# Performance work log

Measured on AMD Instinct MI355X. Metric: run time of the kernel, lower is better.

The kernel has to match this reference:

```python
import jax, jax.numpy as jnp
import numpy as np

B, L, D = 4, 8192, 1024

def setup_inputs() -> dict:
    key = jax.random.key(0)
    kx, kg, kc = jax.random.split(key, 3)
    scale = 1.0 / np.sqrt(D)  # ~xavier for [D,D]
    return {
        "x": jax.random.normal(kx, (B, L, D), dtype=jnp.float32),
        "Wg": jax.random.normal(kg, (D, D), dtype=jnp.float32) * scale,
        "bg": jnp.ones((D,), dtype=jnp.float32),   # gate bias init = 1.0
        "Wc": jax.random.normal(kc, (D, D), dtype=jnp.float32) * scale,
        "bc": jnp.zeros((D,), dtype=jnp.float32),  # candidate bias init = 0
    }

def _mingru_scan(gates, candidates):
    # Linear recurrence h_t = g_t * h_{t-1} + c_t, h_0 = 0, along axis=1 (L).
    # Associative combine for pairs (a, b) representing h -> a*h + b.
    def combine(e1, e2):
        a1, b1 = e1
        a2, b2 = e2
        return a2 * a1, a2 * b1 + b2
    _, h = jax.lax.associative_scan(combine, (gates, candidates), axis=1)
    return h

def reference(x, Wg, bg, Wc, bc):
    # gate_proj / candidate_proj: y = x @ W.T + b (torch Linear convention)
    gates = jax.nn.sigmoid(jnp.einsum('bld,ed->ble', x, Wg) + bg)
    candidates = jnp.tanh(jnp.einsum('bld,ed->ble', x, Wc) + bc)
    return _mingru_scan(gates, candidates)  # dropout=0 -> identity
```

## Files before the change

kernel.cpp:

```cpp
#include <hip/hip_runtime.h>
#include <math.h>

#define B_ 4
#define L_ 8192
#define D_ 1024
#define M_ (B_ * L_)
#define K_ D_

#define BM 128
#define BN 128
#define BK 32

#define NCH 64
#define CHL 128

typedef short bf16x8 __attribute__((ext_vector_type(8)));
typedef float f32x4 __attribute__((ext_vector_type(4)));

__device__ __forceinline__ unsigned short f2bf(float f) {
    unsigned u = __float_as_uint(f);
    u += 0x7fff + ((u >> 16) & 1);
    return (unsigned short)(u >> 16);
}
__device__ __forceinline__ float bf2f(unsigned short h) {
    return __uint_as_float(((unsigned)h) << 16);
}

__device__ __forceinline__ void async16(const void* g, void* l) {
    __builtin_amdgcn_global_load_lds(
        (const __attribute__((address_space(1))) unsigned int*)g,
        (__attribute__((address_space(3))) unsigned int*)l, 16, 0, 0);
}

__global__ __launch_bounds__(256) void wprep_kernel(
    const float* __restrict__ Wg, const float* __restrict__ Wc,
    unsigned short* __restrict__ Wghi, unsigned short* __restrict__ Wglo,
    unsigned short* __restrict__ Wchi, unsigned short* __restrict__ Wclo)
{
    int idx = (blockIdx.x * 256 + threadIdx.x) * 4;
    const int n = D_ * D_;
    const float* src; unsigned short *dh, *dl; int o;
    if (idx < n) { src = Wg; dh = Wghi; dl = Wglo; o = idx; }
    else         { src = Wc; dh = Wchi; dl = Wclo; o = idx - n; }
    float4 v = *(const float4*)(src + o);
    ushort4 hi, lo;
    hi.x = f2bf(v.x); lo.x = f2bf(v.x - bf2f(hi.x));
    hi.y = f2bf(v.y); lo.y = f2bf(v.y - bf2f(hi.y));
    hi.z = f2bf(v.z); lo.z = f2bf(v.z - bf2f(hi.z));
    hi.w = f2bf(v.w); lo.w = f2bf(v.w - bf2f(hi.w));
    *(ushort4*)(dh + o) = hi;
    *(ushort4*)(dl + o) = lo;
}

__global__ __launch_bounds__(256) void xprep_kernel(
    const float* __restrict__ X,
    unsigned short* __restrict__ Xhi, unsigned short* __restrict__ Xlo)
{
    size_t idx = ((size_t)blockIdx.x * 256 + threadIdx.x) * 4;
    float4 v = *(const float4*)(X + idx);
    ushort4 hi, lo;
    hi.x = f2bf(v.x); lo.x = f2bf(v.x - bf2f(hi.x));
    hi.y = f2bf(v.y); lo.y = f2bf(v.y - bf2f(hi.y));
    hi.z = f2bf(v.z); lo.z = f2bf(v.z - bf2f(hi.z));
    hi.w = f2bf(v.w); lo.w = f2bf(v.w - bf2f(hi.w));
    *(ushort4*)(Xhi + idx) = hi;
    *(ushort4*)(Xlo + idx) = lo;
}

__global__ __launch_bounds__(256, 2) void gemm_scan_kernel(
    const unsigned short* __restrict__ Xhi, const unsigned short* __restrict__ Xlo,
    const unsigned short* __restrict__ Wghi, const unsigned short* __restrict__ Wglo,
    const unsigned short* __restrict__ Wchi, const unsigned short* __restrict__ Wclo,
    const float* __restrict__ bg, const float* __restrict__ bc,
    float* __restrict__ P_ws, float* __restrict__ h_ws,
    float* __restrict__ carryA, float* __restrict__ carryB)
{
    __shared__ __align__(16) unsigned short sAhi[BM * BK];
    __shared__ __align__(16) unsigned short sAlo[BM * BK];
    __shared__ __align__(16) unsigned short sB[2][4][BN * BK];

    const int t = threadIdx.x;
    const int lane = t & 63;
    const int w = t >> 6;
    const int wrow = w >> 1;
    const int wcol = w & 1;
    const int quad = lane >> 4;
    const int l16  = lane & 15;

    const int m0 = blockIdx.x * BM;
    const int n0 = blockIdx.y * BN;

    const int stRow = t >> 2;
    const int stKc  = (t & 3) << 3;
    const int stO   = t * 16;

    f32x4 accg[4][4] = {};
    f32x4 accc[4][4] = {};

    unsigned short* sBc = &sB[0][0][0];
    unsigned short* sBn = &sB[1][0][0];

#pragma unroll
    for (int p = 0; p < 2; ++p) {
        const int o = stO + p * 4096;
        const size_t gb = (size_t)(n0 + stRow + p * 64) * K_ + stKc;
        async16(Wghi + gb, (char*)sBc + o);
        async16(Wglo + gb, (char*)sBc + 8192 + o);
        async16(Wchi + gb, (char*)sBc + 16384 + o);
        async16(Wclo + gb, (char*)sBc + 24576 + o);
    }

#pragma unroll 1
    for (int s = 0; s < 32; ++s) {
        const int k0 = s * BK;

        __builtin_amdgcn_s_barrier();

#pragma unroll
        for (int p = 0; p < 2; ++p) {
            const int o = stO + p * 4096;
            const size_t ga = (size_t)(m0 + stRow + p * 64) * K_ + k0 + stKc;
            async16(Xhi + ga, (char*)sAhi + o);
            async16(Xlo + ga, (char*)sAlo + o);
        }

        if (s < 31) {
#pragma unroll
            for (int p = 0; p < 2; ++p) {
                const int o = stO + p * 4096;
                const size_t gb = (size_t)(n0 + stRow + p * 64) * K_ + (k0 + BK) + stKc;
                async16(Wghi + gb, (char*)sBn + o);
                async16(Wglo + gb, (char*)sBn + 8192 + o);
                async16(Wchi + gb, (char*)sBn + 16384 + o);
                async16(Wclo + gb, (char*)sBn + 24576 + o);
            }
            asm volatile("s_waitcnt vmcnt(8)" ::: "memory");
        } else {
            asm volatile("s_waitcnt vmcnt(0)" ::: "memory");
        }
        __builtin_amdgcn_sched_barrier(0);

        __builtin_amdgcn_s_barrier();

        bf16x8 ahi[4], alo[4];
#pragma unroll
        for (int i = 0; i < 4; ++i) {
            const int off = (wrow * 64 + i * 16 + l16) * BK + quad * 8;
            ahi[i] = *(const bf16x8*)(sAhi + off);
            alo[i] = *(const bf16x8*)(sAlo + off);
        }
        __builtin_amdgcn_s_setprio(1);
#pragma unroll
        for (int j = 0; j < 4; ++j) {
            const int off = (wcol * 64 + j * 16 + l16) * BK + quad * 8;
            bf16x8 bgh = *(const bf16x8*)(sBc + off);
            bf16x8 bgl = *(const bf16x8*)(sBc + 4096 + off);
            bf16x8 bch = *(const bf16x8*)(sBc + 8192 + off);
            bf16x8 bcl = *(const bf16x8*)(sBc + 12288 + off);
#pragma unroll
            for (int i = 0; i < 4; ++i) {
                accg[i][j] = __builtin_amdgcn_mfma_f32_16x16x32_bf16(ahi[i], bgh, accg[i][j], 0, 0, 0);
                accg[i][j] = __builtin_amdgcn_mfma_f32_16x16x32_bf16(ahi[i], bgl, accg[i][j], 0, 0, 0);
                accg[i][j] = __builtin_amdgcn_mfma_f32_16x16x32_bf16(alo[i], bgh, accg[i][j], 0, 0, 0);
                accc[i][j] = __builtin_amdgcn_mfma_f32_16x16x32_bf16(ahi[i], bch, accc[i][j], 0, 0, 0);
                accc[i][j] = __builtin_amdgcn_mfma_f32_16x16x32_bf16(ahi[i], bcl, accc[i][j], 0, 0, 0);
                accc[i][j] = __builtin_amdgcn_mfma_f32_16x16x32_bf16(alo[i], bch, accc[i][j], 0, 0, 0);
            }
        }
        __builtin_amdgcn_s_setprio(0);

        unsigned short* tmp = sBc; sBc = sBn; sBn = tmp;
    }

    const int b   = m0 >> 13;
    const int chk = (m0 & (L_ - 1)) >> 7;

    float RunA[4], RunB[4];
#pragma unroll
    for (int j = 0; j < 4; ++j) {
        const int n = n0 + wcol * 64 + j * 16 + l16;
        const float bgv = bg[n];
        const float bcv = bc[n];
        float Ar = 1.f, Br = 0.f;
#pragma unroll
        for (int i = 0; i < 4; ++i) {
            float P[4], H[4];
            float pp = 1.f, ph = 0.f;
#pragma unroll
            for (int r = 0; r < 4; ++r) {
                float zg = accg[i][j][r] + bgv;
                float zc = accc[i][j][r] + bcv;
                float g = 1.f / (1.f + __expf(-zg));
                float c = tanhf(zc);
                float Pv = (r == 0) ? g : g * pp;
                float Hv = (r == 0) ? c : fmaf(g, ph, c);
                P[r] = Pv; H[r] = Hv; pp = Pv; ph = Hv;
            }
            float Ai = P[3], Bi = H[3];
            float A1 = __shfl(Ai, (lane - 16) & 63);
            float B1 = __shfl(Bi, (lane - 16) & 63);
            if (quad >= 1) { Bi = fmaf(Ai, B1, Bi); Ai *= A1; }
            float A2 = __shfl(Ai, (lane - 32) & 63);
            float B2 = __shfl(Bi, (lane - 32) & 63);
            if (quad >= 2) { Bi = fmaf(Ai, B2, Bi); Ai *= A2; }
            float Ae = __shfl(Ai, (lane - 16) & 63);
            float Be = __shfl(Bi, (lane - 16) & 63);
            if (quad == 0) { Ae = 1.f; Be = 0.f; }
            float Ca = Ae * Ar;
            float Cb = fmaf(Ae, Br, Be);
#pragma unroll
            for (int r = 0; r < 4; ++r) {
                float Pr = P[r];
                accg[i][j][r] = Pr * Ca;
                accc[i][j][r] = fmaf(Pr, Cb, H[r]);
            }
            float Ag  = __shfl(Ai, l16 + 48);
            float Bg2 = __shfl(Bi, l16 + 48);
            Br = fmaf(Ag, Br, Bg2);
            Ar *= Ag;
        }
        RunA[j] = Ar; RunB[j] = Br;
    }

    __syncthreads();
    float* cwf = (float*)sAhi;

    if (wrow == 0 && quad == 0) {
#pragma unroll
        for (int j = 0; j < 4; ++j) {
            cwf[(((wcol * 4 + j) * 16 + l16) << 1) + 0] = RunA[j];
            cwf[(((wcol * 4 + j) * 16 + l16) << 1) + 1] = RunB[j];
        }
    }
    __syncthreads();
    if (wrow == 1) {
#pragma unroll
        for (int j = 0; j < 4; ++j) {
            float Aw = cwf[(((wcol * 4 + j) * 16 + l16) << 1) + 0];
            float Bw = cwf[(((wcol * 4 + j) * 16 + l16) << 1) + 1];
#pragma unroll
            for (int i = 0; i < 4; ++i) {
#pragma unroll
                for (int r = 0; r < 4; ++r) {
                    float Pe = accg[i][j][r];
                    accc[i][j][r] = fmaf(Pe, Bw, accc[i][j][r]);
                    accg[i][j][r] = Pe * Aw;
                }
            }
            if (quad == 0) {
                const int n = n0 + wcol * 64 + j * 16 + l16;
                size_t co = (((size_t)b * NCH + chk) << 10) + n;
                carryA[co] = RunA[j] * Aw;
                carryB[co] = fmaf(RunA[j], Bw, RunB[j]);
            }
        }
    }

#pragma unroll
    for (int j = 0; j < 4; ++j) {
        const int n = n0 + wcol * 64 + j * 16 + l16;
#pragma unroll
        for (int i = 0; i < 4; ++i) {
#pragma unroll
            for (int r = 0; r < 4; ++r) {
                int m = m0 + wrow * 64 + i * 16 + quad * 4 + r;
                size_t o = ((size_t)m << 10) + n;
                P_ws[o] = accg[i][j][r];
                h_ws[o] = accc[i][j][r];
            }
        }
    }
}

__global__ __launch_bounds__(256) void scan_carry_kernel(
    const float* __restrict__ carryA, float* __restrict__ carryB)
{
    const int idx = blockIdx.x * 256 + threadIdx.x;
    const int b = idx >> 10;
    const int d = idx & (D_ - 1);
    float acc = 0.f;
    for (int k = 0; k < NCH; ++k) {
        const size_t o = (((size_t)b * NCH + k) << 10) + d;
        const float a  = carryA[o];
        const float bb = carryB[o];
        carryB[o] = acc;
        acc = fmaf(a, acc, bb);
    }
}

__global__ __launch_bounds__(256) void scan_apply_kernel(
    const float* __restrict__ P_ws, const float* __restrict__ h_ws,
    const float* __restrict__ carryB, float* __restrict__ out)
{
    const size_t o = ((size_t)blockIdx.x * 256 + threadIdx.x) * 4;
    const int m  = (int)(o >> 10);
    const int d  = (int)(o & (D_ - 1));
    const int b  = m >> 13;
    const int ch = (m & (L_ - 1)) >> 7;
    const float4 hin = *(const float4*)(carryB + ((((size_t)b * NCH + ch) << 10) + d));
    const float4 P = *(const float4*)(P_ws + o);
    const float4 H = *(const float4*)(h_ws + o);
    float4 r;
    r.x = fmaf(P.x, hin.x, H.x);
    r.y = fmaf(P.y, hin.y, H.y);
    r.z = fmaf(P.z, hin.z, H.z);
    r.w = fmaf(P.w, hin.w, H.w);
    *(float4*)(out + o) = r;
}

extern "C" void kernel_launch(void* const* d_in, const int* in_sizes, int n_in,
                              void* d_out, int out_size, void* d_ws, size_t ws_size,
                              hipStream_t stream)
{
    const float* x  = (const float*)d_in[0];
    const float* Wg = (const float*)d_in[1];
    const float* bg = (const float*)d_in[2];
    const float* Wc = (const float*)d_in[3];
    const float* bc = (const float*)d_in[4];
    float* out = (float*)d_out;

    float* ws = (float*)d_ws;
    float* P_ws   = ws;
    float* h_ws   = P_ws + (size_t)M_ * D_;
    float* carryA = h_ws + (size_t)M_ * D_;
    float* carryB = carryA + (size_t)B_ * NCH * D_;
    unsigned short* Wghi = (unsigned short*)(carryB + (size_t)B_ * NCH * D_);
    unsigned short* Wglo = Wghi + (size_t)D_ * D_;
    unsigned short* Wchi = Wglo + (size_t)D_ * D_;
    unsigned short* Wclo = Wchi + (size_t)D_ * D_;

    unsigned short* Xhi = (unsigned short*)out;
    unsigned short* Xlo = Xhi + (size_t)M_ * D_;

    wprep_kernel<<<(2 * D_ * D_ / 4) / 256, 256, 0, stream>>>(
        Wg, Wc, Wghi, Wglo, Wchi, Wclo);

    xprep_kernel<<<((size_t)M_ * D_ / 4) / 256, 256, 0, stream>>>(x, Xhi, Xlo);

    gemm_scan_kernel<<<dim3(M_ / BM, D_ / BN), 256, 0, stream>>>(
        Xhi, Xlo, Wghi, Wglo, Wchi, Wclo, bg, bc, P_ws, h_ws, carryA, carryB);

    scan_carry_kernel<<<(B_ * D_) / 256, 256, 0, stream>>>(carryA, carryB);

    scan_apply_kernel<<<(M_ * (D_ / 4)) / 256, 256, 0, stream>>>(
        P_ws, h_ws, carryB, out);
}
```

Measured before the change: 727.6 us.

## Load A fragments directly from global into registers with double buffering

After: 849.3 us. +16.7%, slower.

```diff
diff --git a/kernel.cpp b/kernel.cpp
--- a/kernel.cpp
+++ b/kernel.cpp
@@ -75,9 +75,8 @@
     float* __restrict__ P_ws, float* __restrict__ h_ws,
     float* __restrict__ carryA, float* __restrict__ carryB)
 {
-    __shared__ __align__(16) unsigned short sAhi[BM * BK];
-    __shared__ __align__(16) unsigned short sAlo[BM * BK];
-    __shared__ __align__(16) unsigned short sB[2][4][BN * BK];
+    __shared__ __align__(16) unsigned short sB0[4 * BN * BK];
+    __shared__ __align__(16) unsigned short sB1[4 * BN * BK];
 
     const int t = threadIdx.x;
     const int lane = t & 63;
@@ -94,83 +93,86 @@
     const int stKc  = (t & 3) << 3;
     const int stO   = t * 16;
 
+    const size_t aOff = (size_t)(m0 + wrow * 64 + l16) * K_ + quad * 8;
+
     f32x4 accg[4][4] = {};
     f32x4 accc[4][4] = {};
 
-    unsigned short* sBc = &sB[0][0][0];
-    unsigned short* sBn = &sB[1][0][0];
+    bf16x8 A0hi[4], A0lo[4], A1hi[4], A1lo[4];
 
 #pragma unroll
     for (int p = 0; p < 2; ++p) {
         const int o = stO + p * 4096;
         const size_t gb = (size_t)(n0 + stRow + p * 64) * K_ + stKc;
-        async16(Wghi + gb, (char*)sBc + o);
-        async16(Wglo + gb, (char*)sBc + 8192 + o);
-        async16(Wchi + gb, (char*)sBc + 16384 + o);
-        async16(Wclo + gb, (char*)sBc + 24576 + o);
+        async16(Wghi + gb, (char*)sB0 + o);
+        async16(Wglo + gb, (char*)sB0 + 8192 + o);
+        async16(Wchi + gb, (char*)sB0 + 16384 + o);
+        async16(Wclo + gb, (char*)sB0 + 24576 + o);
+    }
+#pragma unroll
+    for (int i = 0; i < 4; ++i) {
+        A0hi[i] = *(const bf16x8*)(Xhi + aOff + (size_t)i * 16 * K_);
+        A0lo[i] = *(const bf16x8*)(Xlo + aOff + (size_t)i * 16 * K_);
+    }
+    __builtin_amdgcn_sched_barrier(0);
+
+#define MFMA_BF16 __builtin_amdgcn_mfma_f32_16x16x32_bf16
+
+#define STEP(s, AHIC, ALOC, AHIN, ALON)                                      \
+    {                                                                        \
+        __builtin_amdgcn_s_barrier();   \
+        if ((s) < 31) {                                                      \
+            const int k1 = ((s) + 1) * BK;                                   \
+            unsigned short* sBn_ = (((s) + 1) & 1) ? sB1 : sB0;              \
+            _Pragma("unroll")                                                \
+            for (int p = 0; p < 2; ++p) {                                    \
+                const int o = stO + p * 4096;                                \
+                const size_t gb = (size_t)(n0 + stRow + p * 64) * K_ + k1 + stKc; \
+                async16(Wghi + gb, (char*)sBn_ + o);                         \
+                async16(Wglo + gb, (char*)sBn_ + 8192 + o);                  \
+                async16(Wchi + gb, (char*)sBn_ + 16384 + o);                 \
+                async16(Wclo + gb, (char*)sBn_ + 24576 + o);                 \
+            }                                                                \
+            _Pragma("unroll")                                                \
+            for (int i = 0; i < 4; ++i) {                                    \
+                AHIN[i] = *(const bf16x8*)(Xhi + aOff + (size_t)i * 16 * K_ + k1); \
+                ALON[i] = *(const bf16x8*)(Xlo + aOff + (size_t)i * 16 * K_ + k1); \
+            }                                                                \
+            asm volatile("s_waitcnt vmcnt(16)" ::: "memory");                \
+        } else {                                                             \
+            asm volatile("s_waitcnt vmcnt(0)" ::: "memory");                 \
+        }                                                                    \
+        __builtin_amdgcn_sched_barrier(0);                                   \
+        __builtin_amdgcn_s_barrier();      \
+        const unsigned short* sBc_ = ((s) & 1) ? sB1 : sB0;                  \
+        __builtin_amdgcn_s_setprio(1);                                       \
+        _Pragma("unroll")                                                    \
+        for (int j = 0; j < 4; ++j) {                                        \
+            const int off = (wcol * 64 + j * 16 + l16) * BK + quad * 8;      \
+            bf16x8 bgh = *(const bf16x8*)(sBc_ + off);                       \
+            bf16x8 bgl = *(const bf16x8*)(sBc_ + 4096 + off);                \
+            bf16x8 bch = *(const bf16x8*)(sBc_ + 8192 + off);                \
+            bf16x8 bcl = *(const bf16x8*)(sBc_ + 12288 + off);               \
+            _Pragma("unroll")                                                \
+            for (int i = 0; i < 4; ++i) {                                    \
+                accg[i][j] = MFMA_BF16(AHIC[i], bgh, accg[i][j], 0, 0, 0);   \
+                accg[i][j] = MFMA_BF16(AHIC[i], bgl, accg[i][j], 0, 0, 0);   \
+                accg[i][j] = MFMA_BF16(ALOC[i], bgh, accg[i][j], 0, 0, 0);   \
+                accc[i][j] = MFMA_BF16(AHIC[i], bch, accc[i][j], 0, 0, 0);   \
+                accc[i][j] = MFMA_BF16(AHIC[i], bcl, accc[i][j], 0, 0, 0);   \
+                accc[i][j] = MFMA_BF16(ALOC[i], bch, accc[i][j], 0, 0, 0);   \
+            }                                                                \
+        }                                                                    \
+        __builtin_amdgcn_s_setprio(0);                                       \
     }
 
 #pragma unroll 1
-    for (int s = 0; s < 32; ++s) {
-        const int k0 = s * BK;
-
-        __builtin_amdgcn_s_barrier();
-
-#pragma unroll
-        for (int p = 0; p < 2; ++p) {
-            const int o = stO + p * 4096;
-            const size_t ga = (size_t)(m0 + stRow + p * 64) * K_ + k0 + stKc;
-            async16(Xhi + ga, (char*)sAhi + o);
-            async16(Xlo + ga, (char*)sAlo + o);
-        }
-
-        if (s < 31) {
-#pragma unroll
-            for (int p = 0; p < 2; ++p) {
-                const int o = stO + p * 4096;
-                const size_t gb = (size_t)(n0 + stRow + p * 64) * K_ + (k0 + BK) + stKc;
-                async16(Wghi + gb, (char*)sBn + o);
-                async16(Wglo + gb, (char*)sBn + 8192 + o);
-                async16(Wchi + gb, (char*)sBn + 16384 + o);
-                async16(Wclo + gb, (char*)sBn + 24576 + o);
-            }
-            asm volatile("s_waitcnt vmcnt(8)" ::: "memory");
-        } else {
-            asm volatile("s_waitcnt vmcnt(0)" ::: "memory");
-        }
-        __builtin_amdgcn_sched_barrier(0);
-
-        __builtin_amdgcn_s_barrier();
-
-        bf16x8 ahi[4], alo[4];
-#pragma unroll
-        for (int i = 0; i < 4; ++i) {
-            const int off = (wrow * 64 + i * 16 + l16) * BK + quad * 8;
-            ahi[i] = *(const bf16x8*)(sAhi + off);
-            alo[i] = *(const bf16x8*)(sAlo + off);
-        }
-        __builtin_amdgcn_s_setprio(1);
-#pragma unroll
-        for (int j = 0; j < 4; ++j) {
-            const int off = (wcol * 64 + j * 16 + l16) * BK + quad * 8;
-            bf16x8 bgh = *(const bf16x8*)(sBc + off);
-            bf16x8 bgl = *(const bf16x8*)(sBc + 4096 + off);
-            bf16x8 bch = *(const bf16x8*)(sBc + 8192 + off);
-            bf16x8 bcl = *(const bf16x8*)(sBc + 12288 + off);
-#pragma unroll
-            for (int i = 0; i < 4; ++i) {
-                accg[i][j] = __builtin_amdgcn_mfma_f32_16x16x32_bf16(ahi[i], bgh, accg[i][j], 0, 0, 0);
-                accg[i][j] = __builtin_amdgcn_mfma_f32_16x16x32_bf16(ahi[i], bgl, accg[i][j], 0, 0, 0);
-                accg[i][j] = __builtin_amdgcn_mfma_f32_16x16x32_bf16(alo[i], bgh, accg[i][j], 0, 0, 0);
-                accc[i][j] = __builtin_amdgcn_mfma_f32_16x16x32_bf16(ahi[i], bch, accc[i][j], 0, 0, 0);
-                accc[i][j] = __builtin_amdgcn_mfma_f32_16x16x32_bf16(ahi[i], bcl, accc[i][j], 0, 0, 0);
-                accc[i][j] = __builtin_amdgcn_mfma_f32_16x16x32_bf16(alo[i], bch, accc[i][j], 0, 0, 0);
-            }
-        }
-        __builtin_amdgcn_s_setprio(0);
-
-        unsigned short* tmp = sBc; sBc = sBn; sBn = tmp;
-    }
+    for (int ss = 0; ss < 16; ++ss) {
+        const int s0 = ss * 2;
+        STEP(s0,     A0hi, A0lo, A1hi, A1lo);
+        STEP(s0 + 1, A1hi, A1lo, A0hi, A0lo);
+    }
+#undef STEP
 
     const int b   = m0 >> 13;
     const int chk = (m0 & (L_ - 1)) >> 7;
@@ -223,7 +225,7 @@
     }
 
     __syncthreads();
-    float* cwf = (float*)sAhi;
+    float* cwf = (float*)sB0;
 
     if (wrow == 0 && quad == 0) {
 #pragma unroll
```
